# Kernel tuning notes

Hardware: AMD Instinct MI355X
Metric: run time of the kernel (lower is better)

The kernel has to match this reference:

```python
import jax, jax.numpy as jnp
import numpy as np
from jax import lax

H = 32  # hidden size (hardcoded in the torch module)

def setup_inputs() -> dict:
    key = jax.random.key(0)
    ks = jax.random.split(key, 7)
    B, T, I = 2048, 512, 64
    s = 1.0 / np.sqrt(H)  # torch nn.LSTM default init scale
    return {
        "x": jax.random.normal(ks[0], (B, T, I), dtype=jnp.float32),
        "W_ih": jax.random.uniform(ks[1], (4 * H, I), jnp.float32, -s, s),
        "W_hh": jax.random.uniform(ks[2], (4 * H, H), jnp.float32, -s, s),
        "b_ih": jax.random.uniform(ks[3], (4 * H,), jnp.float32, -s, s),
        "b_hh": jax.random.uniform(ks[4], (4 * H,), jnp.float32, -s, s),
        "W_fc": jax.random.uniform(ks[5], (1, H), jnp.float32, -s, s),
        "b_fc": jax.random.uniform(ks[6], (1,), jnp.float32, -s, s),
    }

def _lstm_last_h(x, W_ih, W_hh, b_ih, b_hh):
    B = x.shape[0]
    # Precompute input projections for all timesteps: [B, T, 4H] -> [T, B, 4H]
    xg = jnp.einsum('bti,gi->btg', x, W_ih) + (b_ih + b_hh)
    xg = jnp.transpose(xg, (1, 0, 2))

    def step(carry, xt):
        h, c = carry
        g = xt + h @ W_hh.T  # [B, 4H]
        i = jax.nn.sigmoid(g[:, 0 * H:1 * H])
        f = jax.nn.sigmoid(g[:, 1 * H:2 * H])
        gg = jnp.tanh(g[:, 2 * H:3 * H])
        o = jax.nn.sigmoid(g[:, 3 * H:4 * H])
        c = f * c + i * gg
        h = o * jnp.tanh(c)
        return (h, c), None

    init = (jnp.zeros((B, H), x.dtype), jnp.zeros((B, H), x.dtype))
    (h, _), _ = lax.scan(step, init, xg)
    return h  # [B, H], last timestep hidden state

def reference(x, W_ih, W_hh, b_ih, b_hh, W_fc, b_fc):
    # Dropout is identity in eval mode; only the last timestep feeds fc.
    h = _lstm_last_h(x, W_ih, W_hh, b_ih, b_hh)
    return h @ W_fc.T + b_fc  # [B, 1]
```

## Files before the change

### kernel.cpp

```cpp
#include <hip/hip_runtime.h>

typedef __attribute__((ext_vector_type(8))) short short8;
typedef __attribute__((ext_vector_type(4))) float f32x4;

#define LOG2E 1.44269504088896340736f

__device__ __forceinline__ unsigned short f2bf(float f) {
    union { float f; unsigned u; } a; a.f = f;
    unsigned r = a.u + 0x7fffu + ((a.u >> 16) & 1u);
    return (unsigned short)(r >> 16);
}
__device__ __forceinline__ unsigned pk2(float x, float y) {
    return (unsigned)f2bf(x) | ((unsigned)f2bf(y) << 16);
}

__global__ __launch_bounds__(256, 2) void lstm_fused(
    const float* __restrict__ x,
    const float* __restrict__ Wih,
    const float* __restrict__ Whh,
    const float* __restrict__ bih,
    const float* __restrict__ bhh,
    const float* __restrict__ Wfc,
    const float* __restrict__ bfc,
    float* __restrict__ out)
{
    __shared__ unsigned short Wlds[128 * 80];
    __shared__ float xg_sh[4 * 16 * 132];
    __shared__ alignas(64) unsigned short hbuf[4 * 32];

    const int tid  = threadIdx.x;
    const int lane = tid & 63;
    const int wv   = tid >> 6;
    const int b    = blockIdx.x * 4 + wv;
    const int m    = lane & 15;
    const int quad = lane >> 4;

    {
        const float4* w4 = (const float4*)Wih;
        unsigned* wl = (unsigned*)Wlds;
        #pragma unroll
        for (int i = 0; i < 8; i++) {
            int fi = tid * 8 + i;
            int g  = fi >> 4;
            int k  = (fi & 15) << 2;
            float4 v = w4[fi];
            wl[g * 40 + (k >> 1) + 0] = pk2(v.x, v.y);
            wl[g * 40 + (k >> 1) + 1] = pk2(v.z, v.w);
        }
    }

    short8 Bh[8];
    #pragma unroll
    for (int t = 0; t < 8; t++) {
        const float4* wr = (const float4*)(Whh + (size_t)(16 * t + m) * 32 + quad * 8);
        float4 va = wr[0], vb = wr[1];
        union { short8 v; unsigned u[4]; } B;
        B.u[0] = pk2(va.x, va.y); B.u[1] = pk2(va.z, va.w);
        B.u[2] = pk2(vb.x, vb.y); B.u[3] = pk2(vb.z, vb.w);
        Bh[t] = B.v;
    }

    float biasv[8];
    #pragma unroll
    for (int n = 0; n < 8; n++) biasv[n] = bih[16 * n + m] + bhh[16 * n + m];

    const float kmul = (lane < 32) ? 2.0f : 1.0f;
    const float ksub = (lane < 32) ? 1.0f : 0.0f;
    const float kl   = -LOG2E * kmul;
    const bool  q0   = (lane & 16) != 0;
    const bool  q1   = (lane & 32) != 0;
    const bool  lo   = (lane < 32);

    __syncthreads();

    const float* xrow = x + ((size_t)b * 512 + m) * 64;
    float* xgw = xg_sh + wv * 2112;
    unsigned short* hw = hbuf + wv * 32;

    hw[lane & 31] = 0;
    float c = 0.0f, h = 0.0f;
    const f32x4 z4 = {0.f, 0.f, 0.f, 0.f};

    for (int ch = 0; ch < 32; ++ch) {
        const float4* xr4 = (const float4*)(xrow + ch * 1024);
        float4 l0 = xr4[quad * 2];
        float4 l1 = xr4[quad * 2 + 1];
        float4 l2 = xr4[8 + quad * 2];
        float4 l3 = xr4[8 + quad * 2 + 1];
        union { short8 v; unsigned u[4]; } A0, A1;
        A0.u[0] = pk2(l0.x, l0.y); A0.u[1] = pk2(l0.z, l0.w);
        A0.u[2] = pk2(l1.x, l1.y); A0.u[3] = pk2(l1.z, l1.w);
        A1.u[0] = pk2(l2.x, l2.y); A1.u[1] = pk2(l2.z, l2.w);
        A1.u[2] = pk2(l3.x, l3.y); A1.u[3] = pk2(l3.z, l3.w);

        #pragma unroll
        for (int n = 0; n < 8; n++) {
            const short8 B0 = *(const short8*)&Wlds[(16 * n + m) * 80 + quad * 8];
            const short8 B1 = *(const short8*)&Wlds[(16 * n + m) * 80 + 32 + quad * 8];
            f32x4 acc = {0.f, 0.f, 0.f, 0.f};
            acc = __builtin_amdgcn_mfma_f32_16x16x32_bf16(A0.v, B0, acc, 0, 0, 0);
            acc = __builtin_amdgcn_mfma_f32_16x16x32_bf16(A1.v, B1, acc, 0, 0, 0);
            const int pos = ((n & 3) << 5) + 2 * m + (n >> 2);
            #pragma unroll
            for (int r = 0; r < 4; r++)
                xgw[(quad * 4 + r) * 132 + pos] = acc[r] + biasv[n];
        }

        #pragma unroll
        for (int tt = 0; tt < 16; ++tt) {
            const short8 abf = *(const short8*)&hw[quad * 8];
            const f32x4 a0 = __builtin_amdgcn_mfma_f32_16x16x32_bf16(abf, Bh[0], z4, 0, 0, 0);
            const f32x4 a1 = __builtin_amdgcn_mfma_f32_16x16x32_bf16(abf, Bh[1], z4, 0, 0, 0);
            const f32x4 a2 = __builtin_amdgcn_mfma_f32_16x16x32_bf16(abf, Bh[2], z4, 0, 0, 0);
            const f32x4 a3 = __builtin_amdgcn_mfma_f32_16x16x32_bf16(abf, Bh[3], z4, 0, 0, 0);
            const f32x4 a4 = __builtin_amdgcn_mfma_f32_16x16x32_bf16(abf, Bh[4], z4, 0, 0, 0);
            const f32x4 a5 = __builtin_amdgcn_mfma_f32_16x16x32_bf16(abf, Bh[5], z4, 0, 0, 0);
            const f32x4 a6 = __builtin_amdgcn_mfma_f32_16x16x32_bf16(abf, Bh[6], z4, 0, 0, 0);
            const f32x4 a7 = __builtin_amdgcn_mfma_f32_16x16x32_bf16(abf, Bh[7], z4, 0, 0, 0);
            const float hh0 = q1 ? (q0 ? a3[0] : a2[0]) : (q0 ? a1[0] : a0[0]);
            const float hh1 = q1 ? (q0 ? a7[0] : a6[0]) : (q0 ? a5[0] : a4[0]);

            const float2 xg2 = *(const float2*)&xgw[tt * 132 + 2 * lane];
            const float g0 = xg2.x + hh0;
            const float g1 = xg2.y + hh1;

            const float s0 = __builtin_amdgcn_rcpf(1.0f + __builtin_amdgcn_exp2f(-LOG2E * g0));
            const float v1 = __builtin_amdgcn_rcpf(1.0f + __builtin_amdgcn_exp2f(kl * g1));
            const float s1 = fmaf(v1, kmul, -ksub);
            const float f_ = __shfl(s0, lane ^ 32);
            const float o_ = __shfl(s1, lane ^ 32);
            const float ui = lo ? s0 : f_;
            const float vg = lo ? s1 : o_;
            const float wf = lo ? f_ : s0;
            c = fmaf(wf, c, ui * vg);
            const float th = fmaf(2.0f, __builtin_amdgcn_rcpf(
                                 1.0f + __builtin_amdgcn_exp2f(-2.0f * LOG2E * c)), -1.0f);
            const float oo = lo ? o_ : s1;
            h = oo * th;
            hw[lane & 31] = f2bf(h);
        }
    }

    float p = lo ? h * Wfc[lane & 31] : 0.0f;
    #pragma unroll
    for (int msk = 16; msk >= 1; msk >>= 1) p += __shfl_xor(p, msk);
    if (lane == 0) out[b] = p + bfc[0];
}

extern "C" void kernel_launch(void* const* d_in, const int* in_sizes, int n_in,
                              void* d_out, int out_size, void* d_ws, size_t ws_size,
                              hipStream_t stream) {
    const float* x   = (const float*)d_in[0];
    const float* Wih = (const float*)d_in[1];
    const float* Whh = (const float*)d_in[2];
    const float* bih = (const float*)d_in[3];
    const float* bhh = (const float*)d_in[4];
    const float* Wfc = (const float*)d_in[5];
    const float* bfc = (const float*)d_in[6];
    float* out = (float*)d_out;
    lstm_fused<<<dim3(512), dim3(256), 0, stream>>>(x, Wih, Whh, bih, bhh, Wfc, bfc, out);
}
```

Before: 477.2 us.

## Prefetch next x chunk and compute all four gates per lane without shuffles

Loads the next chunk's x rows into registers before the current chunk's MFMA work, so global-load latency overlaps compute. It also changes the xg shared-memory layout so each of the 32 hidden columns reads its four gate preactivations with one float4 load. Each lane now evaluates all four gates directly, which removes the two cross-lane shuffles and selects from the serial recurrence step. The cost is that lanes 32-63 do redundant gate math, and prefetching raises register pressure.

```diff
diff --git a/kernel.cpp b/kernel.cpp
--- a/kernel.cpp
+++ b/kernel.cpp
@@ -12,6 +12,9 @@
 }
 __device__ __forceinline__ unsigned pk2(float x, float y) {
     return (unsigned)f2bf(x) | ((unsigned)f2bf(y) << 16);
+}
+__device__ __forceinline__ float sigm(float x) {
+    return __builtin_amdgcn_rcpf(1.0f + __builtin_amdgcn_exp2f(-LOG2E * x));
 }
 
 __global__ __launch_bounds__(256, 2) void lstm_fused(
@@ -34,6 +37,7 @@
     const int b    = blockIdx.x * 4 + wv;
     const int m    = lane & 15;
     const int quad = lane >> 4;
+    const int cc   = lane & 31;
 
     {
         const float4* w4 = (const float4*)Wih;
@@ -64,12 +68,7 @@
     #pragma unroll
     for (int n = 0; n < 8; n++) biasv[n] = bih[16 * n + m] + bhh[16 * n + m];
 
-    const float kmul = (lane < 32) ? 2.0f : 1.0f;
-    const float ksub = (lane < 32) ? 1.0f : 0.0f;
-    const float kl   = -LOG2E * kmul;
-    const bool  q0   = (lane & 16) != 0;
-    const bool  q1   = (lane & 32) != 0;
-    const bool  lo   = (lane < 32);
+    const bool b4 = (lane & 16) != 0;
 
     __syncthreads();
 
@@ -77,21 +76,30 @@
     float* xgw = xg_sh + wv * 2112;
     unsigned short* hw = hbuf + wv * 32;
 
-    hw[lane & 31] = 0;
+    hw[cc] = 0;
     float c = 0.0f, h = 0.0f;
     const f32x4 z4 = {0.f, 0.f, 0.f, 0.f};
 
+    float4 p0, p1, p2, p3;
+    {
+        const float4* xr4 = (const float4*)xrow;
+        p0 = xr4[quad * 2];     p1 = xr4[quad * 2 + 1];
+        p2 = xr4[8 + quad * 2]; p3 = xr4[8 + quad * 2 + 1];
+    }
+
     for (int ch = 0; ch < 32; ++ch) {
-        const float4* xr4 = (const float4*)(xrow + ch * 1024);
-        float4 l0 = xr4[quad * 2];
-        float4 l1 = xr4[quad * 2 + 1];
-        float4 l2 = xr4[8 + quad * 2];
-        float4 l3 = xr4[8 + quad * 2 + 1];
         union { short8 v; unsigned u[4]; } A0, A1;
-        A0.u[0] = pk2(l0.x, l0.y); A0.u[1] = pk2(l0.z, l0.w);
-        A0.u[2] = pk2(l1.x, l1.y); A0.u[3] = pk2(l1.z, l1.w);
-        A1.u[0] = pk2(l2.x, l2.y); A1.u[1] = pk2(l2.z, l2.w);
-        A1.u[2] = pk2(l3.x, l3.y); A1.u[3] = pk2(l3.z, l3.w);
+        A0.u[0] = pk2(p0.x, p0.y); A0.u[1] = pk2(p0.z, p0.w);
+        A0.u[2] = pk2(p1.x, p1.y); A0.u[3] = pk2(p1.z, p1.w);
+        A1.u[0] = pk2(p2.x, p2.y); A1.u[1] = pk2(p2.z, p2.w);
+        A1.u[2] = pk2(p3.x, p3.y); A1.u[3] = pk2(p3.z, p3.w);
+
+        {
+            const int chn = (ch < 31) ? ch + 1 : 31;
+            const float4* nx = (const float4*)(xrow + (size_t)chn * 1024);
+            p0 = nx[quad * 2];     p1 = nx[quad * 2 + 1];
+            p2 = nx[8 + quad * 2]; p3 = nx[8 + quad * 2 + 1];
+        }
 
         #pragma unroll
         for (int n = 0; n < 8; n++) {
@@ -100,7 +108,7 @@
             f32x4 acc = {0.f, 0.f, 0.f, 0.f};
             acc = __builtin_amdgcn_mfma_f32_16x16x32_bf16(A0.v, B0, acc, 0, 0, 0);
             acc = __builtin_amdgcn_mfma_f32_16x16x32_bf16(A1.v, B1, acc, 0, 0, 0);
-            const int pos = ((n & 3) << 5) + 2 * m + (n >> 2);
+            const int pos = ((n & 1) << 6) + 4 * m + (n >> 1);
             #pragma unroll
             for (int r = 0; r < 4; r++)
                 xgw[(quad * 4 + r) * 132 + pos] = acc[r] + biasv[n];
@@ -117,31 +125,29 @@
             const f32x4 a5 = __builtin_amdgcn_mfma_f32_16x16x32_bf16(abf, Bh[5], z4, 0, 0, 0);
             const f32x4 a6 = __builtin_amdgcn_mfma_f32_16x16x32_bf16(abf, Bh[6], z4, 0, 0, 0);
             const f32x4 a7 = __builtin_amdgcn_mfma_f32_16x16x32_bf16(abf, Bh[7], z4, 0, 0, 0);
-            const float hh0 = q1 ? (q0 ? a3[0] : a2[0]) : (q0 ? a1[0] : a0[0]);
-            const float hh1 = q1 ? (q0 ? a7[0] : a6[0]) : (q0 ? a5[0] : a4[0]);
+            const float hi = b4 ? a1[0] : a0[0];
+            const float hf = b4 ? a3[0] : a2[0];
+            const float hg = b4 ? a5[0] : a4[0];
+            const float ho = b4 ? a7[0] : a6[0];
 
-            const float2 xg2 = *(const float2*)&xgw[tt * 132 + 2 * lane];
-            const float g0 = xg2.x + hh0;
-            const float g1 = xg2.y + hh1;
+            const f32x4 xg4 = *(const f32x4*)&xgw[tt * 132 + 4 * cc];
+            const float gi = xg4[0] + hi;
+            const float gf = xg4[1] + hf;
+            const float gg = xg4[2] + hg;
+            const float go = xg4[3] + ho;
 
-            const float s0 = __builtin_amdgcn_rcpf(1.0f + __builtin_amdgcn_exp2f(-LOG2E * g0));
-            const float v1 = __builtin_amdgcn_rcpf(1.0f + __builtin_amdgcn_exp2f(kl * g1));
-            const float s1 = fmaf(v1, kmul, -ksub);
-            const float f_ = __shfl(s0, lane ^ 32);
-            const float o_ = __shfl(s1, lane ^ 32);
-            const float ui = lo ? s0 : f_;
-            const float vg = lo ? s1 : o_;
-            const float wf = lo ? f_ : s0;
-            c = fmaf(wf, c, ui * vg);
-            const float th = fmaf(2.0f, __builtin_amdgcn_rcpf(
-                                 1.0f + __builtin_amdgcn_exp2f(-2.0f * LOG2E * c)), -1.0f);
-            const float oo = lo ? o_ : s1;
-            h = oo * th;
-            hw[lane & 31] = f2bf(h);
+            const float iv = sigm(gi);
+            const float fv = sigm(gf);
+            const float gv = fmaf(2.0f, sigm(2.0f * gg), -1.0f);
+            const float ov = sigm(go);
+            c = fmaf(fv, c, iv * gv);
+            const float th = fmaf(2.0f, sigm(2.0f * c), -1.0f);
+            h = ov * th;
+            hw[cc] = f2bf(h);
         }
     }
 
-    float p = lo ? h * Wfc[lane & 31] : 0.0f;
+    float p = (lane < 32) ? h * Wfc[cc] : 0.0f;
     #pragma unroll
     for (int msk = 16; msk >= 1; msk >>= 1) p += __shfl_xor(p, msk);
     if (lane == 0) out[b] = p + bfc[0];
```

Result: faster. 431.6 us (-9.6%).
